# Kernel optimization log

Hardware: AMD Instinct MI355X
Metric: run time of the kernel (lower is better)

## Reference

```python
import jax, jax.numpy as jnp
import numpy as np

BETA = 0.25
CODEBOOK_SIZE = 1024
EMB_DIM = 256


def setup_inputs() -> dict:
    key = jax.random.key(0)
    k1, k2 = jax.random.split(key)
    z = jax.random.normal(k1, (32, EMB_DIM, 32, 32), dtype=jnp.float32)  # NCHW
    # torch init: uniform(-1/K, 1/K)
    lim = 1.0 / CODEBOOK_SIZE
    codebook = jax.random.uniform(k2, (CODEBOOK_SIZE, EMB_DIM), dtype=jnp.float32,
                                  minval=-lim, maxval=lim)
    return {"z": z, "codebook": codebook}


def reference(z, codebook):
    # z: [B, C, H, W] -> [B, H, W, C]
    zp = jnp.transpose(z, (0, 2, 3, 1))
    B, H, W, D = zp.shape
    zf = zp.reshape(-1, D)  # [N, D]
    K = codebook.shape[0]

    # pairwise squared distances: ||z||^2 + ||e||^2 - 2 z e^T  -> [N, K]
    d = ((zf * zf).sum(axis=1, keepdims=True)
         + (codebook * codebook).sum(axis=1)
         - 2.0 * jnp.einsum('nd,kd->nk', zf, codebook))
    mean_distance = jnp.mean(d)

    idx = jnp.argmin(d, axis=1)  # [N]
    # direct gather instead of one-hot matmul (same math)
    z_q = codebook[idx].reshape(B, H, W, D)

    loss = (BETA * jnp.mean((jax.lax.stop_gradient(z_q) - zp) ** 2)
            + jnp.mean((z_q - jax.lax.stop_gradient(zp)) ** 2))

    # straight-through estimator
    z_q_st = zp + jax.lax.stop_gradient(z_q - zp)

    # perplexity from mean one-hot usage (bincount via scatter-add)
    N = zf.shape[0]
    counts = jnp.zeros((K,), dtype=zf.dtype).at[idx].add(1.0)
    e_mean = counts / N
    perplexity = jnp.exp(-jnp.sum(e_mean * jnp.log(e_mean + 1e-10)))

    z_q_out = jnp.transpose(z_q_st, (0, 3, 1, 2))  # back to NCHW
    return z_q_out, loss, perplexity, idx, mean_distance
```

## Files before the change

kernel.cpp:

```cpp
#include <hip/hip_runtime.h>
#include <hip/hip_bf16.h>


#define NPTS   32768
#define KCODE  1024
#define DDIM   256
#define HWSZ   1024
#define ZSTRB  262144
#define ZELEMS 8388608

#define OUT_LOSS 8388608
#define OUT_PERP 8388609
#define OUT_IDX  8388610
#define OUT_MD   8421378

#define WS_IDX     0
#define WS_COUNTS  131072
#define WS_RLIST   135168
#define WS_RCOUNT  266240
#define WS_LOSSSUM 266248
#define WS_ZSQ     266256
#define WS_ENSUM   266264
#define WS_CHSUM   266272
#define WS_ESUM    268320
#define WS_ENORM   270368
#define WS_CBT     274464
#define WS_CBHI    1323040
#define WS_CBLO    1847328

#define MARGIN 2e-4f

typedef short  s16x8 __attribute__((ext_vector_type(8)));
typedef unsigned short u16x8 __attribute__((ext_vector_type(8)));
typedef float  f32x4 __attribute__((ext_vector_type(4)));

__device__ __forceinline__ unsigned short bf16_rne(float f) {
    unsigned int u = __float_as_uint(f);
    return (unsigned short)((u + 0x7FFFu + ((u >> 16) & 1u)) >> 16);
}

__global__ __launch_bounds__(256) void init_kernel(char* ws) {
    int t = threadIdx.x;
    int* counts = (int*)(ws + WS_COUNTS);
    for (int i = t; i < 1024; i += 256) counts[i] = 0;
    if (t == 0) *(int*)(ws + WS_RCOUNT) = 0;
    double* dbl = (double*)(ws + WS_LOSSSUM);
    for (int i = t; i < 515; i += 256) dbl[i] = 0.0;
}

__device__ __forceinline__ float np_sumsq256(const float* p) {
    float tot[2];
    #pragma unroll
    for (int h = 0; h < 2; ++h) {
        const float* a = p + h * 128;
        float r[8];
        #pragma unroll
        for (int j = 0; j < 8; ++j) { float v = a[j]; float s = v * v; asm volatile("" : "+v"(s)); r[j] = s; }
        for (int i = 8; i < 128; i += 8) {
            #pragma unroll
            for (int j = 0; j < 8; ++j) { float v = a[i + j]; float s = v * v; asm volatile("" : "+v"(s)); r[j] += s; }
        }
        tot[h] = ((r[0] + r[1]) + (r[2] + r[3])) + ((r[4] + r[5]) + (r[6] + r[7]));
    }
    return tot[0] + tot[1];
}

__global__ __launch_bounds__(256) void prep2_kernel(const float* __restrict__ cb,
                                                    float* __restrict__ enorm,
                                                    float* __restrict__ cbT,
                                                    unsigned short* __restrict__ cbhi,
                                                    unsigned short* __restrict__ cblo,
                                                    double* __restrict__ esum,
                                                    double* __restrict__ enormsum) {
    __shared__ float tile[64][257];
    int t = threadIdx.x;
    int k0 = blockIdx.x * 64;

    for (int i = 0; i < 16; ++i) {
        int f = t + 256 * i;
        int r = f >> 6;
        int c4 = (f & 63) << 2;
        float4 v = *(const float4*)(cb + (size_t)(k0 + r) * DDIM + c4);
        tile[r][c4] = v.x; tile[r][c4 + 1] = v.y; tile[r][c4 + 2] = v.z; tile[r][c4 + 3] = v.w;
    }
    __syncthreads();

    if (t < 64) {
        float s = np_sumsq256(&tile[t][0]);
        enorm[k0 + t] = s;
        double en = (double)s;
        for (int o = 32; o; o >>= 1) en += __shfl_down(en, o, 64);
        if (t == 0) atomicAdd(enormsum, en);
    }

    double cs = 0.0;
    for (int r = 0; r < 64; ++r) cs += (double)tile[r][t];
    atomicAdd(&esum[t], cs);

    {
        int kloc = t & 63, dq = t >> 6;
        for (int dd = 0; dd < 64; ++dd) {
            int d = dd * 4 + dq;
            cbT[(size_t)d * KCODE + k0 + kloc] = tile[kloc][d];
        }
    }

    {
        int row = t >> 2, q = t & 3;
        #pragma unroll
        for (int j = 0; j < 8; ++j) {
            int d0 = q * 64 + j * 8;
            u16x8 H, L;
            #pragma unroll
            for (int e = 0; e < 8; ++e) {
                float f = tile[row][d0 + e];
                unsigned short h = bf16_rne(f);
                H[e] = h;
                L[e] = bf16_rne(f - __uint_as_float((unsigned int)h << 16));
            }
            *(u16x8*)(cbhi + (size_t)(k0 + row) * DDIM + d0) = H;
            *(u16x8*)(cblo + (size_t)(k0 + row) * DDIM + d0) = L;
        }
    }
}

__global__ __launch_bounds__(256, 2) void screen_kernel(const float* __restrict__ z,
                                                        const unsigned short* __restrict__ cbhi,
                                                        const unsigned short* __restrict__ cblo,
                                                        const float* __restrict__ enorm,
                                                        int* __restrict__ ws_idx,
                                                        int* __restrict__ rlist,
                                                        int* __restrict__ rcount) {
    __shared__ unsigned short zhi_lds[64 * DDIM];
    __shared__ unsigned short zlo_lds[64 * DDIM];
    int tid = threadIdx.x;
    int n0 = blockIdx.x * 64;
    int b = n0 >> 10, hw0 = n0 & 1023;
    const float* zb = z + (size_t)b * ZSTRB;
    char* zh = (char*)zhi_lds;
    char* zl = (char*)zlo_lds;

    for (int i = 0; i < 16; ++i) {
        int f = tid + 256 * i;
        int d = f >> 4;
        int p4 = (f & 15) << 2;
        float4 v = *(const float4*)(zb + d * HWSZ + hw0 + p4);
        float vv[4] = {v.x, v.y, v.z, v.w};
        #pragma unroll
        for (int j = 0; j < 4; ++j) {
            int p = p4 + j;
            int off = (p << 9) + (((d << 1)) ^ ((p & 7) << 4));
            unsigned short hi = bf16_rne(vv[j]);
            *(unsigned short*)(zh + off) = hi;
            *(unsigned short*)(zl + off) = bf16_rne(vv[j] - __uint_as_float((unsigned int)hi << 16));
        }
    }
    __syncthreads();

    int lane = tid & 63;
    int w = tid >> 6;
    int col = lane & 15;
    int kq = lane >> 4;
    int rowl = w * 16 + col;
    int swz = (rowl & 7) << 4;

    s16x8 ah[8], al[8];
    #pragma unroll
    for (int kc = 0; kc < 8; ++kc) {
        int off = (rowl << 9) + ((kc * 64 + kq * 16) ^ swz);
        ah[kc] = *(const s16x8*)(zh + off);
        al[kc] = *(const s16x8*)(zl + off);
    }

    float best[4] = {3.4e38f, 3.4e38f, 3.4e38f, 3.4e38f};
    float sec[4]  = {3.4e38f, 3.4e38f, 3.4e38f, 3.4e38f};
    int bidx[4] = {0, 0, 0, 0};

    const char* bhbase = (const char*)cbhi + col * 512 + kq * 16;
    const char* blbase = (const char*)cblo + col * 512 + kq * 16;

    #pragma unroll 1
    for (int chunk = 0; chunk < 64; ++chunk) {
        const char* bh = bhbase + chunk * 8192;
        const char* bl = blbase + chunk * 8192;
        f32x4 hh = {0.f, 0.f, 0.f, 0.f};
        f32x4 hl = {0.f, 0.f, 0.f, 0.f};
        f32x4 lh = {0.f, 0.f, 0.f, 0.f};
        #pragma unroll
        for (int kc = 0; kc < 8; ++kc) {
            s16x8 vbh = *(const s16x8*)(bh + kc * 64);
            s16x8 vbl = *(const s16x8*)(bl + kc * 64);
            hh = __builtin_amdgcn_mfma_f32_16x16x32_bf16(ah[kc], vbh, hh, 0, 0, 0);
            lh = __builtin_amdgcn_mfma_f32_16x16x32_bf16(al[kc], vbh, lh, 0, 0, 0);
            hl = __builtin_amdgcn_mfma_f32_16x16x32_bf16(ah[kc], vbl, hl, 0, 0, 0);
        }
        int k = chunk * 16 + col;
        float ek = enorm[k];
        #pragma unroll
        for (int r = 0; r < 4; ++r) {
            float dot = hh[r] + hl[r] + lh[r];
            float c = fmaf(-2.f, dot, ek);
            if (c < best[r]) { sec[r] = best[r]; best[r] = c; bidx[r] = k; }
            else if (c < sec[r]) sec[r] = c;
        }
    }

    #pragma unroll
    for (int m = 1; m < 16; m <<= 1) {
        #pragma unroll
        for (int r = 0; r < 4; ++r) {
            float ob = __shfl_xor(best[r], m, 64);
            float os = __shfl_xor(sec[r], m, 64);
            int   oi = __shfl_xor(bidx[r], m, 64);
            if (ob < best[r] || (ob == best[r] && oi < bidx[r])) {
                sec[r] = fminf(best[r], os);
                best[r] = ob; bidx[r] = oi;
            } else {
                sec[r] = fminf(sec[r], ob);
            }
        }
    }

    if (col == 0) {
        #pragma unroll
        for (int r = 0; r < 4; ++r) {
            int n = n0 + w * 16 + kq * 4 + r;
            ws_idx[n] = bidx[r];
            if (sec[r] - best[r] < MARGIN) {
                int slot = atomicAdd(rcount, 1);
                if (slot < NPTS) rlist[slot] = n;
            }
        }
    }
}

__global__ __launch_bounds__(256) void recheck_kernel(const float* __restrict__ z,
                                                      const float* __restrict__ cbT,
                                                      const float* __restrict__ enorm,
                                                      int* __restrict__ ws_idx,
                                                      const int* __restrict__ rlist,
                                                      const int* __restrict__ rcount) {
    __shared__ float zs[DDIM];
    __shared__ float s_sh;
    __shared__ float bv[256];
    __shared__ int   bi[256];
    int t = threadIdx.x;
    int cnt = *rcount; if (cnt > NPTS) cnt = NPTS;
    for (int it = blockIdx.x; it < cnt; it += gridDim.x) {
        int n = rlist[it];
        int b = n >> 10, hw = n & 1023;
        zs[t] = z[(size_t)b * ZSTRB + (size_t)t * HWSZ + hw];
        __syncthreads();
        if (t == 0) s_sh = np_sumsq256(zs);
        __syncthreads();
        float s_n = s_sh;
        float best = 3.4e38f; int bidx = 0;
        #pragma unroll
        for (int j = 0; j < 4; ++j) {
            int k = t + 256 * j;
            double dot = 0.0;
            for (int d = 0; d < DDIM; ++d)
                dot = fma((double)cbT[d * KCODE + k], (double)zs[d], dot);
            float E = (float)dot;
            float w = 2.0f * E;
            float u = s_n + enorm[k];
            float dd = u - w;
            if (dd < best) { best = dd; bidx = k; }
        }
        bv[t] = best; bi[t] = bidx;
        __syncthreads();
        for (int s2 = 128; s2; s2 >>= 1) {
            if (t < s2) {
                if (bv[t + s2] < bv[t] || (bv[t + s2] == bv[t] && bi[t + s2] < bi[t])) {
                    bv[t] = bv[t + s2]; bi[t] = bi[t + s2];
                }
            }
            __syncthreads();
        }
        if (t == 0) ws_idx[n] = bi[0];
        __syncthreads();
    }
}

__global__ __launch_bounds__(256) void hist_kernel(const int* __restrict__ ws_idx,
                                                   int* __restrict__ counts,
                                                   float* __restrict__ out_idx) {
    __shared__ int h[KCODE];
    int t = threadIdx.x;
    for (int i = t; i < KCODE; i += 256) h[i] = 0;
    __syncthreads();
    int n = blockIdx.x * 256 + t;
    int idx = ws_idx[n];
    out_idx[n] = (float)idx;
    atomicAdd(&h[idx], 1);
    __syncthreads();
    for (int i = t; i < KCODE; i += 256) { int c = h[i]; if (c) atomicAdd(&counts[i], c); }
}

__global__ __launch_bounds__(256) void out_kernel(const float* __restrict__ z,
                                                  const float* __restrict__ cb,
                                                  const int* __restrict__ ws_idx,
                                                  float* __restrict__ out,
                                                  double* __restrict__ lossSum,
                                                  double* __restrict__ chsum,
                                                  double* __restrict__ zsq) {
    int t = threadIdx.x;
    size_t base = (size_t)blockIdx.x * 1024;
    int c = blockIdx.x & 255;
    int b = blockIdx.x >> 8;
    int hw = t * 4;
    const float4 zv = *(const float4*)(z + base + hw);
    int4 iv = *(const int4*)(ws_idx + b * HWSZ + hw);
    float q0 = cb[(size_t)iv.x * DDIM + c];
    float q1 = cb[(size_t)iv.y * DDIM + c];
    float q2 = cb[(size_t)iv.z * DDIM + c];
    float q3 = cb[(size_t)iv.w * DDIM + c];
    float t0 = q0 - zv.x, t1 = q1 - zv.y, t2 = q2 - zv.z, t3 = q3 - zv.w;
    float4 o; o.x = zv.x + t0; o.y = zv.y + t1; o.z = zv.z + t2; o.w = zv.w + t3;
    *(float4*)(out + base + hw) = o;

    double ls  = (double)t0 * t0 + (double)t1 * t1 + (double)t2 * t2 + (double)t3 * t3;
    double zs  = (double)zv.x + (double)zv.y + (double)zv.z + (double)zv.w;
    double zq2 = (double)zv.x * zv.x + (double)zv.y * zv.y + (double)zv.z * zv.z + (double)zv.w * zv.w;

    __shared__ double r1[4], r2[4], r3[4];
    for (int o2 = 32; o2; o2 >>= 1) {
        ls  += __shfl_down(ls,  o2, 64);
        zs  += __shfl_down(zs,  o2, 64);
        zq2 += __shfl_down(zq2, o2, 64);
    }
    if ((t & 63) == 0) { int w = t >> 6; r1[w] = ls; r2[w] = zs; r3[w] = zq2; }
    __syncthreads();
    if (t == 0) {
        atomicAdd(lossSum, r1[0] + r1[1] + r1[2] + r1[3]);
        atomicAdd(&chsum[c], r2[0] + r2[1] + r2[2] + r2[3]);
        atomicAdd(zsq, r3[0] + r3[1] + r3[2] + r3[3]);
    }
}

__global__ __launch_bounds__(256) void fin_kernel(const int* __restrict__ counts,
                                                  const double* __restrict__ lossSum,
                                                  const double* __restrict__ chsum,
                                                  const double* __restrict__ esum,
                                                  const double* __restrict__ zsq,
                                                  const double* __restrict__ enormsum,
                                                  float* __restrict__ out) {
    int t = threadIdx.x;
    double ent = 0.0;
    for (int i = t; i < KCODE; i += 256) {
        float em = (float)counts[i] / 32768.0f;
        ent += (double)(em * logf(em + 1e-10f));
    }
    double pd = chsum[t] * esum[t];

    __shared__ double r1[4], r2[4];
    for (int o2 = 32; o2; o2 >>= 1) {
        ent += __shfl_down(ent, o2, 64);
        pd  += __shfl_down(pd,  o2, 64);
    }
    if ((t & 63) == 0) { int w = t >> 6; r1[w] = ent; r2[w] = pd; }
    __syncthreads();
    if (t == 0) {
        double ENT = r1[0] + r1[1] + r1[2] + r1[3];
        double PD  = r2[0] + r2[1] + r2[2] + r2[3];
        float m = (float)(*lossSum / (double)ZELEMS);
        out[OUT_LOSS] = 0.25f * m + m;
        out[OUT_PERP] = expf((float)(-ENT));
        double md = *zsq / (double)NPTS + *enormsum / (double)KCODE
                    - (2.0 / ((double)NPTS * (double)KCODE)) * PD;
        out[OUT_MD] = (float)md;
    }
}

extern "C" void kernel_launch(void* const* d_in, const int* in_sizes, int n_in,
                              void* d_out, int out_size, void* d_ws, size_t ws_size,
                              hipStream_t stream) {
    const float* z  = (const float*)d_in[0];
    const float* cb = (const float*)d_in[1];
    float* out = (float*)d_out;
    char* ws = (char*)d_ws;

    int*    ws_idx   = (int*)(ws + WS_IDX);
    int*    counts   = (int*)(ws + WS_COUNTS);
    int*    rlist    = (int*)(ws + WS_RLIST);
    int*    rcount   = (int*)(ws + WS_RCOUNT);
    double* lossSum  = (double*)(ws + WS_LOSSSUM);
    double* zsq      = (double*)(ws + WS_ZSQ);
    double* enormsum = (double*)(ws + WS_ENSUM);
    double* chsum    = (double*)(ws + WS_CHSUM);
    double* esum     = (double*)(ws + WS_ESUM);
    float*  enorm    = (float*)(ws + WS_ENORM);
    float*  cbT      = (float*)(ws + WS_CBT);
    unsigned short* cbhi = (unsigned short*)(ws + WS_CBHI);
    unsigned short* cblo = (unsigned short*)(ws + WS_CBLO);

    hipLaunchKernelGGL(init_kernel, dim3(1), dim3(256), 0, stream, ws);
    hipLaunchKernelGGL(prep2_kernel, dim3(16), dim3(256), 0, stream,
                       cb, enorm, cbT, cbhi, cblo, esum, enormsum);
    hipLaunchKernelGGL(screen_kernel, dim3(512), dim3(256), 0, stream,
                       z, cbhi, cblo, enorm, ws_idx, rlist, rcount);
    hipLaunchKernelGGL(recheck_kernel, dim3(256), dim3(256), 0, stream,
                       z, cbT, enorm, ws_idx, rlist, rcount);
    hipLaunchKernelGGL(hist_kernel, dim3(128), dim3(256), 0, stream,
                       ws_idx, counts, out + OUT_IDX);
    hipLaunchKernelGGL(out_kernel, dim3(8192), dim3(256), 0, stream,
                       z, cb, ws_idx, out, lossSum, chsum, zsq);
    hipLaunchKernelGGL(fin_kernel, dim3(1), dim3(256), 0, stream,
                       counts, lossSum, chsum, esum, zsq, enormsum, out);
}
```

Measured before the change: 780.1 us.

## Drop z low-part MFMA in screen, load z directly, widen prep and recheck grids

The screening kernel no longer stages z into LDS as bf16 hi/lo pairs. It converts z to bf16 straight from global memory into registers and drops the al*bh MFMA product, so each chunk issues two MFMAs instead of three. To cover the added error, the recheck margin grows from 2e-4 to 3e-4, and occupancy is raised to 4 blocks per SM. Codebook prep is split over 64 blocks of 16 rows instead of 16 blocks of 64, the recheck grid doubles, and the fp64 recheck dot uses four independent accumulators. The strided, uncoalesced z loads and a larger set of rechecked points could offset the savings.

```diff
diff --git a/kernel.cpp b/kernel.cpp
--- a/kernel.cpp
+++ b/kernel.cpp
@@ -28,7 +28,7 @@
 #define WS_CBHI    1323040
 #define WS_CBLO    1847328
 
-#define MARGIN 2e-4f
+#define MARGIN 3e-4f
 
 typedef short  s16x8 __attribute__((ext_vector_type(8)));
 typedef unsigned short u16x8 __attribute__((ext_vector_type(8)));
@@ -72,11 +72,12 @@
                                                     unsigned short* __restrict__ cblo,
                                                     double* __restrict__ esum,
                                                     double* __restrict__ enormsum) {
-    __shared__ float tile[64][257];
-    int t = threadIdx.x;
-    int k0 = blockIdx.x * 64;
-
-    for (int i = 0; i < 16; ++i) {
+    __shared__ float tile[16][257];
+    int t = threadIdx.x;
+    int k0 = blockIdx.x * 16;
+
+    #pragma unroll
+    for (int i = 0; i < 4; ++i) {
         int f = t + 256 * i;
         int r = f >> 6;
         int c4 = (f & 63) << 2;
@@ -85,91 +86,71 @@
     }
     __syncthreads();
 
-    if (t < 64) {
+    if (t < 16) {
         float s = np_sumsq256(&tile[t][0]);
         enorm[k0 + t] = s;
         double en = (double)s;
-        for (int o = 32; o; o >>= 1) en += __shfl_down(en, o, 64);
+        for (int o = 8; o; o >>= 1) en += __shfl_down(en, o, 64);
         if (t == 0) atomicAdd(enormsum, en);
     }
 
     double cs = 0.0;
-    for (int r = 0; r < 64; ++r) cs += (double)tile[r][t];
+    for (int r = 0; r < 16; ++r) cs += (double)tile[r][t];
     atomicAdd(&esum[t], cs);
 
     {
-        int kloc = t & 63, dq = t >> 6;
-        for (int dd = 0; dd < 64; ++dd) {
-            int d = dd * 4 + dq;
+        int kloc = t & 15, dg = t >> 4;
+        #pragma unroll
+        for (int dd = 0; dd < 16; ++dd) {
+            int d = dd * 16 + dg;
             cbT[(size_t)d * KCODE + k0 + kloc] = tile[kloc][d];
         }
     }
 
     {
-        int row = t >> 2, q = t & 3;
-        #pragma unroll
-        for (int j = 0; j < 8; ++j) {
-            int d0 = q * 64 + j * 8;
+        int row = t >> 4;
+        int d0 = (t & 15) * 16;
+        #pragma unroll
+        for (int j = 0; j < 2; ++j) {
             u16x8 H, L;
             #pragma unroll
             for (int e = 0; e < 8; ++e) {
-                float f = tile[row][d0 + e];
+                float f = tile[row][d0 + j * 8 + e];
                 unsigned short h = bf16_rne(f);
                 H[e] = h;
                 L[e] = bf16_rne(f - __uint_as_float((unsigned int)h << 16));
             }
-            *(u16x8*)(cbhi + (size_t)(k0 + row) * DDIM + d0) = H;
-            *(u16x8*)(cblo + (size_t)(k0 + row) * DDIM + d0) = L;
-        }
-    }
-}
-
-__global__ __launch_bounds__(256, 2) void screen_kernel(const float* __restrict__ z,
+            *(u16x8*)(cbhi + (size_t)(k0 + row) * DDIM + d0 + j * 8) = H;
+            *(u16x8*)(cblo + (size_t)(k0 + row) * DDIM + d0 + j * 8) = L;
+        }
+    }
+}
+
+__global__ __launch_bounds__(256, 4) void screen_kernel(const float* __restrict__ z,
                                                         const unsigned short* __restrict__ cbhi,
                                                         const unsigned short* __restrict__ cblo,
                                                         const float* __restrict__ enorm,
                                                         int* __restrict__ ws_idx,
                                                         int* __restrict__ rlist,
                                                         int* __restrict__ rcount) {
-    __shared__ unsigned short zhi_lds[64 * DDIM];
-    __shared__ unsigned short zlo_lds[64 * DDIM];
     int tid = threadIdx.x;
     int n0 = blockIdx.x * 64;
     int b = n0 >> 10, hw0 = n0 & 1023;
-    const float* zb = z + (size_t)b * ZSTRB;
-    char* zh = (char*)zhi_lds;
-    char* zl = (char*)zlo_lds;
-
-    for (int i = 0; i < 16; ++i) {
-        int f = tid + 256 * i;
-        int d = f >> 4;
-        int p4 = (f & 15) << 2;
-        float4 v = *(const float4*)(zb + d * HWSZ + hw0 + p4);
-        float vv[4] = {v.x, v.y, v.z, v.w};
-        #pragma unroll
-        for (int j = 0; j < 4; ++j) {
-            int p = p4 + j;
-            int off = (p << 9) + (((d << 1)) ^ ((p & 7) << 4));
-            unsigned short hi = bf16_rne(vv[j]);
-            *(unsigned short*)(zh + off) = hi;
-            *(unsigned short*)(zl + off) = bf16_rne(vv[j] - __uint_as_float((unsigned int)hi << 16));
-        }
-    }
-    __syncthreads();
-
     int lane = tid & 63;
     int w = tid >> 6;
     int col = lane & 15;
     int kq = lane >> 4;
-    int rowl = w * 16 + col;
-    int swz = (rowl & 7) << 4;
-
-    s16x8 ah[8], al[8];
+
+    const float* zp = z + (size_t)b * ZSTRB + (hw0 + w * 16 + col);
+    s16x8 ah[8];
     #pragma unroll
     for (int kc = 0; kc < 8; ++kc) {
-        int off = (rowl << 9) + ((kc * 64 + kq * 16) ^ swz);
-        ah[kc] = *(const s16x8*)(zh + off);
-        al[kc] = *(const s16x8*)(zl + off);
+        u16x8 H;
+        #pragma unroll
+        for (int e = 0; e < 8; ++e)
+            H[e] = bf16_rne(zp[(size_t)(kc * 32 + kq * 8 + e) << 10]);
+        union { u16x8 u; s16x8 s; } cvt; cvt.u = H;
+        ah[kc] = cvt.s;
     }
 
     float best[4] = {3.4e38f, 3.4e38f, 3.4e38f, 3.4e38f};
@@ -185,20 +166,18 @@
         const char* bl = blbase + chunk * 8192;
         f32x4 hh = {0.f, 0.f, 0.f, 0.f};
         f32x4 hl = {0.f, 0.f, 0.f, 0.f};
-        f32x4 lh = {0.f, 0.f, 0.f, 0.f};
         #pragma unroll
         for (int kc = 0; kc < 8; ++kc) {
             s16x8 vbh = *(const s16x8*)(bh + kc * 64);
             s16x8 vbl = *(const s16x8*)(bl + kc * 64);
             hh = __builtin_amdgcn_mfma_f32_16x16x32_bf16(ah[kc], vbh, hh, 0, 0, 0);
-            lh = __builtin_amdgcn_mfma_f32_16x16x32_bf16(al[kc], vbh, lh, 0, 0, 0);
             hl = __builtin_amdgcn_mfma_f32_16x16x32_bf16(ah[kc], vbl, hl, 0, 0, 0);
         }
         int k = chunk * 16 + col;
         float ek = enorm[k];
         #pragma unroll
         for (int r = 0; r < 4; ++r) {
-            float dot = hh[r] + hl[r] + lh[r];
+            float dot = hh[r] + hl[r];
             float c = fmaf(-2.f, dot, ek);
             if (c < best[r]) { sec[r] = best[r]; best[r] = c; bidx[r] = k; }
             else if (c < sec[r]) sec[r] = c;
@@ -258,9 +237,14 @@
         #pragma unroll
         for (int j = 0; j < 4; ++j) {
             int k = t + 256 * j;
-            double dot = 0.0;
-            for (int d = 0; d < DDIM; ++d)
-                dot = fma((double)cbT[d * KCODE + k], (double)zs[d], dot);
+            double a0 = 0.0, a1 = 0.0, a2 = 0.0, a3 = 0.0;
+            for (int d = 0; d < DDIM; d += 4) {
+                a0 = fma((double)cbT[(d + 0) * KCODE + k], (double)zs[d + 0], a0);
+                a1 = fma((double)cbT[(d + 1) * KCODE + k], (double)zs[d + 1], a1);
+                a2 = fma((double)cbT[(d + 2) * KCODE + k], (double)zs[d + 2], a2);
+                a3 = fma((double)cbT[(d + 3) * KCODE + k], (double)zs[d + 3], a3);
+            }
+            double dot = (a0 + a1) + (a2 + a3);
             float E = (float)dot;
             float w = 2.0f * E;
             float u = s_n + enorm[k];
@@ -395,11 +379,11 @@
     unsigned short* cblo = (unsigned short*)(ws + WS_CBLO);
 
     hipLaunchKernelGGL(init_kernel, dim3(1), dim3(256), 0, stream, ws);
-    hipLaunchKernelGGL(prep2_kernel, dim3(16), dim3(256), 0, stream,
+    hipLaunchKernelGGL(prep2_kernel, dim3(64), dim3(256), 0, stream,
                        cb, enorm, cbT, cbhi, cblo, esum, enormsum);
     hipLaunchKernelGGL(screen_kernel, dim3(512), dim3(256), 0, stream,
                        z, cbhi, cblo, enorm, ws_idx, rlist, rcount);
-    hipLaunchKernelGGL(recheck_kernel, dim3(256), dim3(256), 0, stream,
+    hipLaunchKernelGGL(recheck_kernel, dim3(512), dim3(256), 0, stream,
                        z, cbT, enorm, ws_idx, rlist, rcount);
     hipLaunchKernelGGL(hist_kernel, dim3(128), dim3(256), 0, stream,
                        ws_idx, counts, out + OUT_IDX);
```

Result: slower. 802.6 us (+2.9%).
